# Kernel optimization log

Hardware: AMD Instinct MI355X
Metric: run time of the kernel (lower is better)

Reference implementation:

```python
import jax, jax.numpy as jnp
import numpy as np

LN_EPS = 1e-5

def _layer_norm(x, gamma, beta):
    mu = jnp.mean(x, axis=-1, keepdims=True)
    var = jnp.mean(jnp.square(x - mu), axis=-1, keepdims=True)
    return (x - mu) * jax.lax.rsqrt(var + LN_EPS) * gamma + beta

def setup_inputs() -> dict:
    key = jax.random.key(0)
    ks = jax.random.split(key, 6)
    B, Lc, S, H = 8, 16384, 2048, 256
    char_embeddings = jax.random.normal(ks[0], (B, Lc, H), dtype=jnp.float32)
    # include some negative indices (-1, -2) to exercise the no-token mask path
    token_alignment = jax.random.randint(ks[1], (B, Lc), -2, S, dtype=jnp.int32).astype(jnp.int64)
    decoder_hidden_states = jax.random.normal(ks[2], (B, S, H), dtype=jnp.float32)
    scale1 = 1.0 / np.sqrt(2 * H)
    W1 = jax.random.normal(ks[3], (2 * H, H), dtype=jnp.float32) * scale1
    b1 = jnp.zeros((H,), dtype=jnp.float32)
    W2 = jax.random.normal(ks[4], (2 * H, H), dtype=jnp.float32) * scale1
    b2 = jnp.zeros((H,), dtype=jnp.float32)
    ln_gamma = jnp.ones((H,), dtype=jnp.float32)
    ln_beta = jnp.zeros((H,), dtype=jnp.float32)
    return {
        "char_embeddings": char_embeddings,
        "token_alignment": token_alignment,
        "decoder_hidden_states": decoder_hidden_states,
        "W1": W1, "b1": b1, "W2": W2, "b2": b2,
        "ln_gamma": ln_gamma, "ln_beta": ln_beta,
    }

def reference(char_embeddings, token_alignment, decoder_hidden_states,
              W1, b1, W2, b2, ln_gamma, ln_beta):
    B, Lc, H = char_embeddings.shape
    S = decoder_hidden_states.shape[1]
    # per-character gather of decoder token representations (vectorized over batch)
    valid_idx = jnp.clip(token_alignment, 0, S - 1)                         # [B, Lc]
    tok_reprs = jnp.take_along_axis(decoder_hidden_states,
                                    valid_idx[..., None].astype(jnp.int32),
                                    axis=1)                                  # [B, Lc, H]
    tok_reprs = jnp.where((token_alignment < 0)[..., None], 0.0, tok_reprs)
    # alignment_network: Linear(2H -> H)
    combined = jnp.concatenate([char_embeddings, tok_reprs], axis=-1)        # [B, Lc, 2H]
    aligned = jnp.einsum('blk,kh->blh', combined, W1) + b1                   # [B, Lc, H]
    # syllable_feature_extractor: Linear(2H->H) + LayerNorm + GELU (+ eval-mode Dropout)
    combined2 = jnp.concatenate([char_embeddings, aligned], axis=-1)         # [B, Lc, 2H]
    feats = jnp.einsum('blk,kh->blh', combined2, W2) + b2
    feats = _layer_norm(feats, ln_gamma, ln_beta)
    feats = jax.nn.gelu(feats, approximate=False)                            # torch nn.GELU exact
    return char_embeddings + feats
```

## Files before the change

### kernel.cpp

```cpp
#include <hip/hip_runtime.h>
#include <hip/hip_bf16.h>
#include <math.h>
#include <stdint.h>

#define H     256
#define K2    512
#define SDEC  2048
#define LCSH  14
#define BM    64
#define NTHR  256

typedef __attribute__((ext_vector_type(8))) short  short8;
typedef __attribute__((ext_vector_type(4))) float  f32x4;

__device__ __forceinline__ unsigned short f2bf(float f) {
  union { float f; unsigned int u; } c; c.f = f;
  unsigned int u = c.u;
  unsigned int r = u + 0x7fffu + ((u >> 16) & 1u);
  return (unsigned short)(r >> 16);
}

__global__ __launch_bounds__(256) void fuse_weights(
    const float* __restrict__ W1, const float* __restrict__ W2,
    const float* __restrict__ b1, const float* __restrict__ b2,
    unsigned short* __restrict__ wft, float* __restrict__ biasf) {
  if (blockIdx.x == 32) {
    const int n = threadIdx.x;
    float a0 = b2[n], a1 = 0.f, a2 = 0.f, a3 = 0.f;
#pragma unroll 4
    for (int j = 0; j < H; j += 4) {
      a0 += b1[j + 0] * W2[(size_t)(H + j + 0) * H + n];
      a1 += b1[j + 1] * W2[(size_t)(H + j + 1) * H + n];
      a2 += b1[j + 2] * W2[(size_t)(H + j + 2) * H + n];
      a3 += b1[j + 3] * W2[(size_t)(H + j + 3) * H + n];
    }
    biasf[n] = (a0 + a1) + (a2 + a3);
    return;
  }

  __shared__ float As[64][65];
  __shared__ float Bs[64][65];
  const int t  = threadIdx.x;
  const int k0 = (blockIdx.x >> 2) * 64;
  const int n0 = (blockIdx.x & 3) * 64;
  const int lr = t >> 2;
  const int ls = t & 3;
  const int tk = t >> 4;
  const int tn = t & 15;

  float acc[4][4];
#pragma unroll
  for (int i = 0; i < 4; ++i)
#pragma unroll
    for (int c = 0; c < 4; ++c) acc[i][c] = 0.0f;

  for (int jt = 0; jt < 4; ++jt) {
    const int j0 = jt * 64;
    __syncthreads();
    const float* a_src = W1 + (size_t)(k0 + lr) * H + j0 + ls * 16;
    const float* b_src = W2 + (size_t)(H + j0 + lr) * H + n0 + ls * 16;
#pragma unroll
    for (int i = 0; i < 16; ++i) {
      As[lr][ls * 16 + i] = a_src[i];
      Bs[lr][ls * 16 + i] = b_src[i];
    }
    __syncthreads();
#pragma unroll 8
    for (int j = 0; j < 64; ++j) {
      float a[4], b[4];
#pragma unroll
      for (int i = 0; i < 4; ++i) a[i] = As[tk * 4 + i][j];
#pragma unroll
      for (int c = 0; c < 4; ++c) b[c] = Bs[j][tn * 4 + c];
#pragma unroll
      for (int i = 0; i < 4; ++i)
#pragma unroll
        for (int c = 0; c < 4; ++c) acc[i][c] += a[i] * b[c];
    }
  }

#pragma unroll
  for (int i = 0; i < 4; ++i) {
    const int k  = k0 + tk * 4 + i;
    const int kk = k >> 5;
    const int qv = (k >> 3) & 3;
    const int e  = k & 7;
#pragma unroll
    for (int c = 0; c < 4; ++c) {
      const int n = n0 + tn * 4 + c;
      float v = acc[i][c];
      if (k < H) v += W2[(size_t)k * H + n];
      const int n16 = n >> 4;
      const int l15 = n & 15;
      wft[(size_t)(n16 * 16 + kk) * 512 + (qv * 16 + l15) * 8 + e] = f2bf(v);
    }
  }
}

__global__ __launch_bounds__(NTHR, 3) void syl_main(
    const float* __restrict__ cemb, const int* __restrict__ tal,
    const float* __restrict__ dec, const unsigned short* __restrict__ wft,
    const float* __restrict__ biasf, const float* __restrict__ gamma,
    const float* __restrict__ beta, float* __restrict__ out) {

  const int t    = threadIdx.x;
  const int wave = t >> 6;
  const int lane = t & 63;
  const int q    = lane >> 4;
  const int l15  = lane & 15;

  const int nwg  = gridDim.x;
  const int bid  = ((nwg & 7) == 0)
                     ? (int)((blockIdx.x & 7) * (nwg >> 3) + (blockIdx.x >> 3))
                     : (int)blockIdx.x;
  const int row0 = bid * BM;
  const int bidx = row0 >> LCSH;

  const int arow = row0 + wave * 16 + l15;
  int ix = tal[arow];
  const float msk = (ix < 0) ? 0.0f : 1.0f;
  ix = ix < 0 ? 0 : (ix >= SDEC ? SDEC - 1 : ix);

  const float* __restrict__ ap = cemb + (size_t)arow * H + q * 8;
  const float* __restrict__ dp = dec + ((size_t)bidx * SDEC + ix) * H + q * 8;
  const unsigned short* __restrict__ wp = wft + (size_t)lane * 8;

  f32x4 acc[16];
#pragma unroll
  for (int n = 0; n < 16; ++n) acc[n] = (f32x4){0.f, 0.f, 0.f, 0.f};

#pragma unroll 2
  for (int kk = 0; kk < 8; ++kk) {
    const float4 a0 = *(const float4*)(ap + kk * 32);
    const float4 a1 = *(const float4*)(ap + kk * 32 + 4);
    unsigned short hb[8];
    hb[0] = f2bf(a0.x); hb[1] = f2bf(a0.y); hb[2] = f2bf(a0.z); hb[3] = f2bf(a0.w);
    hb[4] = f2bf(a1.x); hb[5] = f2bf(a1.y); hb[6] = f2bf(a1.z); hb[7] = f2bf(a1.w);
    const short8 af = *(const short8*)hb;
#pragma unroll
    for (int h = 0; h < 2; ++h) {
      short8 bf[8];
#pragma unroll
      for (int n = 0; n < 8; ++n)
        bf[n] = *(const short8*)(wp + (size_t)((h * 8 + n) * 16 + kk) * 512);
#pragma unroll
      for (int n = 0; n < 8; ++n)
        acc[h * 8 + n] = __builtin_amdgcn_mfma_f32_16x16x32_bf16(
            af, bf[n], acc[h * 8 + n], 0, 0, 0);
    }
  }

#pragma unroll 2
  for (int kk = 0; kk < 8; ++kk) {
    float4 a0 = *(const float4*)(dp + kk * 32);
    float4 a1 = *(const float4*)(dp + kk * 32 + 4);
    a0.x *= msk; a0.y *= msk; a0.z *= msk; a0.w *= msk;
    a1.x *= msk; a1.y *= msk; a1.z *= msk; a1.w *= msk;
    unsigned short hb[8];
    hb[0] = f2bf(a0.x); hb[1] = f2bf(a0.y); hb[2] = f2bf(a0.z); hb[3] = f2bf(a0.w);
    hb[4] = f2bf(a1.x); hb[5] = f2bf(a1.y); hb[6] = f2bf(a1.z); hb[7] = f2bf(a1.w);
    const short8 af = *(const short8*)hb;
#pragma unroll
    for (int h = 0; h < 2; ++h) {
      short8 bf[8];
#pragma unroll
      for (int n = 0; n < 8; ++n)
        bf[n] = *(const short8*)(wp + (size_t)((h * 8 + n) * 16 + kk + 8) * 512);
#pragma unroll
      for (int n = 0; n < 8; ++n)
        acc[h * 8 + n] = __builtin_amdgcn_mfma_f32_16x16x32_bf16(
            af, bf[n], acc[h * 8 + n], 0, 0, 0);
    }
  }

  float bv[16], gv[16], bev[16];
#pragma unroll
  for (int n = 0; n < 16; ++n) {
    bv[n]  = biasf[n * 16 + l15];
    gv[n]  = gamma[n * 16 + l15];
    bev[n] = beta [n * 16 + l15];
  }

#pragma unroll
  for (int r = 0; r < 4; ++r) {
    float a = 0.f, b2s = 0.f;
#pragma unroll
    for (int n = 0; n < 16; ++n) {
      const float v = acc[n][r] + bv[n];
      acc[n][r] = v;
      a += v; b2s += v * v;
    }
#pragma unroll
    for (int d = 1; d < 16; d <<= 1) {
      a   += __shfl_xor(a, d, 64);
      b2s += __shfl_xor(b2s, d, 64);
    }
    const float mu   = a * (1.0f / 256.0f);
    const float var  = b2s * (1.0f / 256.0f) - mu * mu;
    const float rstd = rsqrtf(var + 1e-5f);

    const size_t ro = ((size_t)row0 + wave * 16 + q * 4 + r) * H + l15;
    const float* __restrict__ cr = cemb + ro;
    float* __restrict__ orow = out + ro;

    float res[16];
#pragma unroll
    for (int n = 0; n < 16; ++n) res[n] = cr[n * 16];
#pragma unroll
    for (int n = 0; n < 16; ++n) {
      const float x = (acc[n][r] - mu) * rstd;
      const float y = x * gv[n] + bev[n];
      const float g = 0.5f * y * (1.0f + erff(y * 0.70710678118654752f));
      orow[n * 16] = res[n] + g;
    }
  }
}

extern "C" void kernel_launch(void* const* d_in, const int* in_sizes, int n_in,
                              void* d_out, int out_size, void* d_ws, size_t ws_size,
                              hipStream_t stream) {
  const float* cemb  = (const float*)d_in[0];
  const int*   tal   = (const int*)d_in[1];
  const float* dec   = (const float*)d_in[2];
  const float* W1    = (const float*)d_in[3];
  const float* b1    = (const float*)d_in[4];
  const float* W2    = (const float*)d_in[5];
  const float* b2    = (const float*)d_in[6];
  const float* gamma = (const float*)d_in[7];
  const float* beta  = (const float*)d_in[8];
  float* out = (float*)d_out;

  unsigned short* wft = (unsigned short*)d_ws;
  float* biasf = (float*)((char*)d_ws + (size_t)K2 * H * sizeof(unsigned short));

  const int rows = in_sizes[0] / H;

  hipLaunchKernelGGL(fuse_weights, dim3(33), dim3(256), 0, stream,
                     W1, W2, b1, b2, wft, biasf);
  hipLaunchKernelGGL(syl_main, dim3(rows / BM), dim3(NTHR), 0, stream,
                     cemb, tal, dec, wft, biasf, gamma, beta, out);
}
```

Before: 407.5 us.

## Split output columns across wave pairs, use hardware bf16 pack and fast GELU

Each 256-thread block now covers 32 rows instead of 64. Two waves share each 16-row slab, and each wave computes half of the 256 output columns, which halves its accumulator registers so occupancy can rise to 4 blocks per CU. The two halves of each LayerNorm row reduction are combined through shared memory behind a barrier. Input conversion uses the v_cvt_pk_bf16_f32 instruction, and exact erf GELU is replaced with a polynomial erf approximation (Abramowitz–Stegun style), which adds a small accuracy risk.

```diff
diff --git a/kernel.cpp b/kernel.cpp
--- a/kernel.cpp
+++ b/kernel.cpp
@@ -7,7 +7,7 @@
 #define K2    512
 #define SDEC  2048
 #define LCSH  14
-#define BM    64
+#define BMR   32
 #define NTHR  256
 
 typedef __attribute__((ext_vector_type(8))) short  short8;
@@ -18,6 +18,25 @@
   unsigned int u = c.u;
   unsigned int r = u + 0x7fffu + ((u >> 16) & 1u);
   return (unsigned short)(r >> 16);
+}
+
+__device__ __forceinline__ short8 pack_bf16x8(float4 a0, float4 a1) {
+  union { unsigned int u[4]; short8 s; } r;
+  asm("v_cvt_pk_bf16_f32 %0, %1, %2" : "=v"(r.u[0]) : "v"(a0.x), "v"(a0.y));
+  asm("v_cvt_pk_bf16_f32 %0, %1, %2" : "=v"(r.u[1]) : "v"(a0.z), "v"(a0.w));
+  asm("v_cvt_pk_bf16_f32 %0, %1, %2" : "=v"(r.u[2]) : "v"(a1.x), "v"(a1.y));
+  asm("v_cvt_pk_bf16_f32 %0, %1, %2" : "=v"(r.u[3]) : "v"(a1.z), "v"(a1.w));
+  return r.s;
+}
+
+__device__ __forceinline__ float fast_gelu(float y) {
+  const float s  = y * 0.70710678118654752f;
+  const float ax = fabsf(s);
+  const float tt = __builtin_amdgcn_rcpf(1.0f + 0.47047f * ax);
+  const float e  = __expf(-ax * ax);
+  const float p  = tt * (0.3480242f + tt * (-0.0958798f + tt * 0.7478556f));
+  const float er = copysignf(1.0f - p * e, s);
+  return 0.5f * y * (1.0f + er);
 }
 
 __global__ __launch_bounds__(256) void fuse_weights(
@@ -97,57 +116,55 @@
   }
 }
 
-__global__ __launch_bounds__(NTHR, 3) void syl_main(
+__global__ __launch_bounds__(NTHR, 4) void syl_main(
     const float* __restrict__ cemb, const int* __restrict__ tal,
     const float* __restrict__ dec, const unsigned short* __restrict__ wft,
     const float* __restrict__ biasf, const float* __restrict__ gamma,
     const float* __restrict__ beta, float* __restrict__ out) {
+
+  __shared__ float st[4][16][2];
 
   const int t    = threadIdx.x;
   const int wave = t >> 6;
   const int lane = t & 63;
   const int q    = lane >> 4;
   const int l15  = lane & 15;
+  const int rw   = wave >> 1;
+  const int ch   = wave & 1;
 
   const int nwg  = gridDim.x;
   const int bid  = ((nwg & 7) == 0)
                      ? (int)((blockIdx.x & 7) * (nwg >> 3) + (blockIdx.x >> 3))
                      : (int)blockIdx.x;
-  const int row0 = bid * BM;
+  const int row0 = bid * BMR;
   const int bidx = row0 >> LCSH;
 
-  const int arow = row0 + wave * 16 + l15;
+  const int arow = row0 + rw * 16 + l15;
   int ix = tal[arow];
   const float msk = (ix < 0) ? 0.0f : 1.0f;
   ix = ix < 0 ? 0 : (ix >= SDEC ? SDEC - 1 : ix);
 
   const float* __restrict__ ap = cemb + (size_t)arow * H + q * 8;
   const float* __restrict__ dp = dec + ((size_t)bidx * SDEC + ix) * H + q * 8;
-  const unsigned short* __restrict__ wp = wft + (size_t)lane * 8;
-
-  f32x4 acc[16];
-#pragma unroll
-  for (int n = 0; n < 16; ++n) acc[n] = (f32x4){0.f, 0.f, 0.f, 0.f};
+  const unsigned short* __restrict__ wp =
+      wft + (size_t)(ch * 8 * 16) * 512 + (size_t)lane * 8;
+
+  f32x4 acc[8];
+#pragma unroll
+  for (int n = 0; n < 8; ++n) acc[n] = (f32x4){0.f, 0.f, 0.f, 0.f};
 
 #pragma unroll 2
   for (int kk = 0; kk < 8; ++kk) {
     const float4 a0 = *(const float4*)(ap + kk * 32);
     const float4 a1 = *(const float4*)(ap + kk * 32 + 4);
-    unsigned short hb[8];
-    hb[0] = f2bf(a0.x); hb[1] = f2bf(a0.y); hb[2] = f2bf(a0.z); hb[3] = f2bf(a0.w);
-    hb[4] = f2bf(a1.x); hb[5] = f2bf(a1.y); hb[6] = f2bf(a1.z); hb[7] = f2bf(a1.w);
-    const short8 af = *(const short8*)hb;
-#pragma unroll
-    for (int h = 0; h < 2; ++h) {
-      short8 bf[8];
-#pragma unroll
-      for (int n = 0; n < 8; ++n)
-        bf[n] = *(const short8*)(wp + (size_t)((h * 8 + n) * 16 + kk) * 512);
-#pragma unroll
-      for (int n = 0; n < 8; ++n)
-        acc[h * 8 + n] = __builtin_amdgcn_mfma_f32_16x16x32_bf16(
-            af, bf[n], acc[h * 8 + n], 0, 0, 0);
-    }
+    const short8 af = pack_bf16x8(a0, a1);
+    short8 bf[8];
+#pragma unroll
+    for (int n = 0; n < 8; ++n)
+      bf[n] = *(const short8*)(wp + (size_t)(n * 16 + kk) * 512);
+#pragma unroll
+    for (int n = 0; n < 8; ++n)
+      acc[n] = __builtin_amdgcn_mfma_f32_16x16x32_bf16(af, bf[n], acc[n], 0, 0, 0);
   }
 
 #pragma unroll 2
@@ -156,36 +173,30 @@
     float4 a1 = *(const float4*)(dp + kk * 32 + 4);
     a0.x *= msk; a0.y *= msk; a0.z *= msk; a0.w *= msk;
     a1.x *= msk; a1.y *= msk; a1.z *= msk; a1.w *= msk;
-    unsigned short hb[8];
-    hb[0] = f2bf(a0.x); hb[1] = f2bf(a0.y); hb[2] = f2bf(a0.z); hb[3] = f2bf(a0.w);
-    hb[4] = f2bf(a1.x); hb[5] = f2bf(a1.y); hb[6] = f2bf(a1.z); hb[7] = f2bf(a1.w);
-    const short8 af = *(const short8*)hb;
-#pragma unroll
-    for (int h = 0; h < 2; ++h) {
-      short8 bf[8];
-#pragma unroll
-      for (int n = 0; n < 8; ++n)
-        bf[n] = *(const short8*)(wp + (size_t)((h * 8 + n) * 16 + kk + 8) * 512);
-#pragma unroll
-      for (int n = 0; n < 8; ++n)
-        acc[h * 8 + n] = __builtin_amdgcn_mfma_f32_16x16x32_bf16(
-            af, bf[n], acc[h * 8 + n], 0, 0, 0);
-    }
-  }
-
-  float bv[16], gv[16], bev[16];
-#pragma unroll
-  for (int n = 0; n < 16; ++n) {
-    bv[n]  = biasf[n * 16 + l15];
-    gv[n]  = gamma[n * 16 + l15];
-    bev[n] = beta [n * 16 + l15];
+    const short8 af = pack_bf16x8(a0, a1);
+    short8 bf[8];
+#pragma unroll
+    for (int n = 0; n < 8; ++n)
+      bf[n] = *(const short8*)(wp + (size_t)(n * 16 + kk + 8) * 512);
+#pragma unroll
+    for (int n = 0; n < 8; ++n)
+      acc[n] = __builtin_amdgcn_mfma_f32_16x16x32_bf16(af, bf[n], acc[n], 0, 0, 0);
+  }
+
+  float bv[8], gv[8], bev[8];
+#pragma unroll
+  for (int n = 0; n < 8; ++n) {
+    const int col = ch * 128 + n * 16 + l15;
+    bv[n]  = biasf[col];
+    gv[n]  = gamma[col];
+    bev[n] = beta [col];
   }
 
 #pragma unroll
   for (int r = 0; r < 4; ++r) {
     float a = 0.f, b2s = 0.f;
 #pragma unroll
-    for (int n = 0; n < 16; ++n) {
+    for (int n = 0; n < 8; ++n) {
       const float v = acc[n][r] + bv[n];
       acc[n][r] = v;
       a += v; b2s += v * v;
@@ -195,23 +206,34 @@
       a   += __shfl_xor(a, d, 64);
       b2s += __shfl_xor(b2s, d, 64);
     }
+    if (l15 == 0) {
+      st[wave][q * 4 + r][0] = a;
+      st[wave][q * 4 + r][1] = b2s;
+    }
+  }
+  __syncthreads();
+
+#pragma unroll
+  for (int r = 0; r < 4; ++r) {
+    const int row = q * 4 + r;
+    const float a   = st[wave][row][0] + st[wave ^ 1][row][0];
+    const float b2s = st[wave][row][1] + st[wave ^ 1][row][1];
     const float mu   = a * (1.0f / 256.0f);
     const float var  = b2s * (1.0f / 256.0f) - mu * mu;
     const float rstd = rsqrtf(var + 1e-5f);
 
-    const size_t ro = ((size_t)row0 + wave * 16 + q * 4 + r) * H + l15;
+    const size_t ro = ((size_t)row0 + rw * 16 + row) * H + ch * 128 + l15;
     const float* __restrict__ cr = cemb + ro;
     float* __restrict__ orow = out + ro;
 
-    float res[16];
-#pragma unroll
-    for (int n = 0; n < 16; ++n) res[n] = cr[n * 16];
-#pragma unroll
-    for (int n = 0; n < 16; ++n) {
+    float res[8];
+#pragma unroll
+    for (int n = 0; n < 8; ++n) res[n] = cr[n * 16];
+#pragma unroll
+    for (int n = 0; n < 8; ++n) {
       const float x = (acc[n][r] - mu) * rstd;
       const float y = x * gv[n] + bev[n];
-      const float g = 0.5f * y * (1.0f + erff(y * 0.70710678118654752f));
-      orow[n * 16] = res[n] + g;
+      orow[n * 16] = res[n] + fast_gelu(y);
     }
   }
 }
@@ -237,6 +259,6 @@
 
   hipLaunchKernelGGL(fuse_weights, dim3(33), dim3(256), 0, stream,
                      W1, W2, b1, b2, wft, biasf);
-  hipLaunchKernelGGL(syl_main, dim3(rows / BM), dim3(NTHR), 0, stream,
+  hipLaunchKernelGGL(syl_main, dim3(rows / BMR), dim3(NTHR), 0, stream,
                      cemb, tal, dec, wft, biasf, gamma, beta, out);
 }
```

Result: faster. 393.0 us (-3.6%).
